# Kernel tuning notes

Measured on AMD Instinct MI355X. Metric: run time of the kernel, lower is better.

## Reference

```python
import jax, jax.numpy as jnp
import numpy as np

B, T, I, H = 128, 128, 12, 512


def setup_inputs() -> dict:
    key = jax.random.key(0)
    k1, k2, k3, k4 = jax.random.split(key, 4)
    s_ih = 1.0 / np.sqrt(H)
    return {
        "history": jax.random.normal(k1, (B, T, I), dtype=jnp.float32),
        "W_ih": jax.random.uniform(k2, (3 * H, I), dtype=jnp.float32, minval=-s_ih, maxval=s_ih),
        "W_hh": jax.random.uniform(k3, (3 * H, H), dtype=jnp.float32, minval=-s_ih, maxval=s_ih),
        "W_pred": jax.random.uniform(k4, (2, H), dtype=jnp.float32, minval=-s_ih, maxval=s_ih),
    }


def reference(history, W_ih, W_hh, W_pred):
    # GRUCell (bias=False), PyTorch gate order: r, z, n
    def step(h, x_t):
        gi = x_t @ W_ih.T            # [B, 3H]
        gh = h @ W_hh.T              # [B, 3H]
        i_r, i_z, i_n = jnp.split(gi, 3, axis=-1)
        h_r, h_z, h_n = jnp.split(gh, 3, axis=-1)
        r = jax.nn.sigmoid(i_r + h_r)
        z = jax.nn.sigmoid(i_z + h_z)
        n = jnp.tanh(i_n + r * h_n)
        h_new = (1.0 - z) * n + z * h
        logit = h_new @ W_pred.T     # per-step bubble_prediction head
        return h_new, logit

    h0 = jnp.zeros((history.shape[0], W_hh.shape[1]), dtype=history.dtype)
    xs = jnp.swapaxes(history, 0, 1)          # [T, B, I]
    h_last, logits_tbf = jax.lax.scan(step, h0, xs)
    logits = jnp.swapaxes(logits_tbf, 0, 1)   # [B, T, 2]
    return logits, h_last
```

## Files before the change

kernel.cpp:

```cpp
#include <hip/hip_runtime.h>
#include <cstdint>


typedef __attribute__((ext_vector_type(4))) float f32x4;
typedef __attribute__((ext_vector_type(8))) __bf16 bf16x8;

#define NTHREADS 256
#define CG_N 32
#define BB 16
#define HC 16
#define T_STEPS 128
#define I_DIM 12
#define H_DIM 512

#define WS_HX0   0
#define WS_HX1   262144
#define WS_FLAGS 524288

__device__ __forceinline__ float bf16f(unsigned short u){
  return __uint_as_float(((unsigned int)u) << 16);
}
__device__ __forceinline__ void split_bf16(float x, unsigned short &hi, unsigned short &lo){
  unsigned int u = __float_as_uint(x);
  hi = (unsigned short)(u >> 16);
  float r = x - __uint_as_float((u >> 16) << 16);
  unsigned int ru = __float_as_uint(r);
  ru += 0x7fffu + ((ru >> 16) & 1u);
  lo = (unsigned short)(ru >> 16);
}
__device__ __forceinline__ float fsigmoid(float x){ return 1.0f / (1.0f + __expf(-x)); }
__device__ __forceinline__ float ftanh(float x){ return 2.0f / (1.0f + __expf(-2.0f * x)) - 1.0f; }
__device__ __forceinline__ f32x4 MFMA(bf16x8 a, bf16x8 b, f32x4 c){
  return __builtin_amdgcn_mfma_f32_16x16x32_bf16(a, b, c, 0, 0, 0);
}
__device__ __forceinline__ void wait_vm0(){
  asm volatile("s_waitcnt vmcnt(0)" ::: "memory");
}
__device__ __forceinline__ unsigned int hiP(unsigned int x, unsigned int y){
  return (x >> 16) | (y & 0xFFFF0000u);
}
__device__ __forceinline__ unsigned int loP(unsigned int x, unsigned int y){
  return (x & 0xFFFFu) | (y << 16);
}

__device__ __forceinline__ void bar_lgkm(){
  asm volatile("s_waitcnt lgkmcnt(0)" ::: "memory");
  __builtin_amdgcn_sched_barrier(0);
  __builtin_amdgcn_s_barrier();
  __builtin_amdgcn_sched_barrier(0);
}
__device__ __forceinline__ void bar_raw(){
  __builtin_amdgcn_sched_barrier(0);
  __builtin_amdgcn_s_barrier();
  __builtin_amdgcn_sched_barrier(0);
}

__device__ __forceinline__ void dev_store_u32(unsigned int* p, unsigned int v){
  asm volatile("global_store_dword %0, %1, off sc1" :: "v"(p), "v"(v) : "memory");
}
__device__ __forceinline__ unsigned int dev_load_u32(const unsigned int* p){
  unsigned int v;
  asm volatile("global_load_dword %0, %1, off sc1\n\ts_waitcnt vmcnt(0)"
               : "=v"(v) : "v"(p) : "memory");
  return v;
}
__device__ __forceinline__ uint4 load4_sc1(const unsigned int* p){
  uint4 v;
  asm volatile("global_load_dwordx4 %0, %1, off sc1" : "=v"(v) : "v"(p) : "memory");
  return v;
}
__device__ __forceinline__ void load_h_row(const unsigned int* p, uint4* pr){
  uint4 v0, v1, v2, v3, v4, v5, v6, v7;
  asm volatile(
    "global_load_dwordx4 %0, %8, off sc1\n\t"
    "global_load_dwordx4 %1, %8, off offset:16 sc1\n\t"
    "global_load_dwordx4 %2, %8, off offset:32 sc1\n\t"
    "global_load_dwordx4 %3, %8, off offset:48 sc1\n\t"
    "global_load_dwordx4 %4, %8, off offset:64 sc1\n\t"
    "global_load_dwordx4 %5, %8, off offset:80 sc1\n\t"
    "global_load_dwordx4 %6, %8, off offset:96 sc1\n\t"
    "global_load_dwordx4 %7, %8, off offset:112 sc1\n\t"
    "s_waitcnt vmcnt(0)"
    : "=&v"(v0), "=&v"(v1), "=&v"(v2), "=&v"(v3),
      "=&v"(v4), "=&v"(v5), "=&v"(v6), "=&v"(v7)
    : "v"(p) : "memory");
  pr[0]=v0; pr[1]=v1; pr[2]=v2; pr[3]=v3; pr[4]=v4; pr[5]=v5; pr[6]=v6; pr[7]=v7;
}

__device__ __forceinline__ void poll_h_row(const unsigned int* p, uint4* pr,
                                           unsigned int want){
  for (;;){
    load_h_row(p, pr);
    unsigned int diff = 0u;
    #pragma unroll
    for (int b = 0; b < 8; ++b)
      diff |= (pr[b].x ^ want) | (pr[b].y ^ want) | (pr[b].z ^ want) | (pr[b].w ^ want);
    if ((diff & 3u) == 0u) break;
  }
  #pragma unroll
  for (int b = 0; b < 8; ++b){
    pr[b].x &= 0xFFFFFFFCu; pr[b].y &= 0xFFFFFFFCu;
    pr[b].z &= 0xFFFFFFFCu; pr[b].w &= 0xFFFFFFFCu;
  }
}

extern "C" __global__ void __launch_bounds__(NTHREADS, 1)
gru_persistent(const float* __restrict__ hist, const float* __restrict__ wih,
               const float* __restrict__ whh, const float* __restrict__ wpred,
               float* __restrict__ out, unsigned char* __restrict__ ws)
{
  __shared__ __align__(16) unsigned short whi_l[3*16*64*8];
  __shared__ __align__(16) unsigned short wlo_l[3*16*64*8];
  __shared__ __align__(16) unsigned short hhi_l[BB*H_DIM];
  __shared__ __align__(16) unsigned short hlo_l[BB*H_DIM];
  __shared__ __align__(16) float part_l[4*3*64*4];
  __shared__ __align__(16) float x_l[BB*I_DIM];
  __shared__ __align__(16) float wih_l[48*I_DIM];
  __shared__ __align__(16) float wpred_l[2*H_DIM];

  const int tid  = threadIdx.x;
  const int bg   = blockIdx.x & 7;
  const int cg   = blockIdx.x >> 3;
  const int wave = tid >> 6;
  const int lane = tid & 63;
  const int b_log = cg & 15;
  const int o_log = cg >> 4;

  unsigned int* hx[2] = {(unsigned int*)(ws + WS_HX0), (unsigned int*)(ws + WS_HX1)};
  unsigned int* flagsP = (unsigned int*)(ws + WS_FLAGS);

  for (int i = tid; i < 48*I_DIM; i += NTHREADS){
    int j = i / I_DIM, ii = i % I_DIM;
    int R = (j >> 4)*H_DIM + cg*HC + (j & 15);
    wih_l[i] = wih[R*I_DIM + ii];
  }
  for (int i = tid; i < 2*H_DIM; i += NTHREADS) wpred_l[i] = wpred[i];
  #pragma unroll
  for (int it = 0; it < 24; ++it){
    int f0 = (it*NTHREADS + tid) * 4;
    int j = f0 >> 9, k = f0 & 511;
    int R = (j >> 4)*H_DIM + cg*HC + (j & 15);
    float4 v = *(const float4*)(whh + R*H_DIM + k);
    int nt = j >> 4;
    int ln = (j & 15) | (((k >> 3) & 3) << 4);
    int kt = k >> 5, e = k & 7;
    int base = (((nt*16 + kt)*64) + ln)*8 + e;
    float vv[4] = {v.x, v.y, v.z, v.w};
    unsigned short h4[4], l4[4];
    #pragma unroll
    for (int q = 0; q < 4; ++q) split_bf16(vv[q], h4[q], l4[q]);
    uint2 uh, ul;
    uh.x = (unsigned int)h4[0] | ((unsigned int)h4[1] << 16);
    uh.y = (unsigned int)h4[2] | ((unsigned int)h4[3] << 16);
    ul.x = (unsigned int)l4[0] | ((unsigned int)l4[1] << 16);
    ul.y = (unsigned int)l4[2] | ((unsigned int)l4[3] << 16);
    *(uint2*)((char*)whi_l + base*2) = uh;
    *(uint2*)((char*)wlo_l + base*2) = ul;
  }

  {
    int b = tid >> 4, hc = tid & 15;
    int gidx = (bg*BB + b)*H_DIM + cg*HC + hc;
    dev_store_u32(hx[0] + gidx, 0u);
    dev_store_u32(hx[1] + gidx, 2u);
  }
  wait_vm0();
  __syncthreads();
  if (wave == 0 && lane < CG_N)
    dev_store_u32(flagsP + (bg*CG_N + lane)*CG_N + cg, 1u);
  if (wave == 0){
    const unsigned int* fp = flagsP + (bg*CG_N + cg)*CG_N + (lane & 31);
    for (;;){
      unsigned int f = dev_load_u32(fp);
      if (__ballot(f >= 1u) == ~0ull) break;
      __builtin_amdgcn_s_sleep(1);
    }
  }
  __syncthreads();

  for (int t = 0; t < T_STEPS; ++t){
    const int cur = t & 1, nxt = cur ^ 1;

    if (tid < BB*I_DIM){
      int b = tid / I_DIM, ii = tid % I_DIM;
      x_l[tid] = hist[((bg*BB + b)*T_STEPS + t)*I_DIM + ii];
    }

    {
      int row = tid & 15, col0 = (tid >> 4) * 32;
      const unsigned int* p = hx[cur] + (bg*BB + row)*H_DIM + col0;
      uint4 pr[8];
      poll_h_row(p, pr, (unsigned int)(t & 3));
      #pragma unroll
      for (int k = 0; k < 4; ++k){
        uint4 a = pr[2*k], b = pr[2*k+1];
        uint4 hi4 = { hiP(a.x,a.y), hiP(a.z,a.w), hiP(b.x,b.y), hiP(b.z,b.w) };
        uint4 lo4 = { loP(a.x,a.y), loP(a.z,a.w), loP(b.x,b.y), loP(b.z,b.w) };
        int boff = row*1024 + (((col0 + 8*k)*2) ^ ((row & 7) << 4));
        *(uint4*)((char*)hhi_l + boff) = hi4;
        *(uint4*)((char*)hlo_l + boff) = lo4;
      }
    }
    bar_lgkm();

    f32x4 acc[3];
    #pragma unroll
    for (int nt = 0; nt < 3; ++nt) acc[nt] = {0.f, 0.f, 0.f, 0.f};
    #pragma unroll
    for (int kk = 0; kk < 4; ++kk){
      int kt = wave*4 + kk;
      int arow = lane & 15;
      int aboff = arow*1024 + ((kt*64 + (lane >> 4)*16) ^ ((arow & 7) << 4));
      bf16x8 ahi = *(const bf16x8*)((const char*)hhi_l + aboff);
      bf16x8 alo = *(const bf16x8*)((const char*)hlo_l + aboff);
      #pragma unroll
      for (int nt = 0; nt < 3; ++nt){
        int bboff = (((nt*16 + kt)*64) + lane)*16;
        bf16x8 bhi = *(const bf16x8*)((const char*)whi_l + bboff);
        bf16x8 blo = *(const bf16x8*)((const char*)wlo_l + bboff);
        acc[nt] = MFMA(ahi, bhi, acc[nt]);
        acc[nt] = MFMA(ahi, blo, acc[nt]);
        acc[nt] = MFMA(alo, bhi, acc[nt]);
      }
    }
    #pragma unroll
    for (int nt = 0; nt < 3; ++nt)
      *(f32x4*)(part_l + ((wave*3 + nt)*64 + lane)*4) = acc[nt];
    bar_lgkm();

    {
      int b = tid >> 4, hc = tid & 15;
      int lc = ((b >> 2) << 4) | hc;
      int rc = b & 3;
      float gh[3];
      #pragma unroll
      for (int g = 0; g < 3; ++g){
        float s = 0.f;
        #pragma unroll
        for (int w = 0; w < 4; ++w) s += part_l[((w*3 + g)*64 + lc)*4 + rc];
        gh[g] = s;
      }
      float gi[3];
      #pragma unroll
      for (int g = 0; g < 3; ++g){
        float s = 0.f;
        #pragma unroll
        for (int ii = 0; ii < I_DIM; ++ii)
          s += x_l[b*I_DIM + ii] * wih_l[(g*16 + hc)*I_DIM + ii];
        gi[g] = s;
      }
      float r = fsigmoid(gi[0] + gh[0]);
      float z = fsigmoid(gi[1] + gh[1]);
      float n = ftanh(gi[2] + r*gh[2]);
      int colg = cg*HC + hc;
      int hoff = b*1024 + ((colg*2) ^ ((b & 7) << 4));
      float hp = bf16f(*(unsigned short*)((char*)hhi_l + hoff))
               + bf16f(*(unsigned short*)((char*)hlo_l + hoff));
      float hn = (1.0f - z)*n + z*hp;

      unsigned short shi, slo; split_bf16(hn, shi, slo);
      unsigned int pk = ((unsigned int)shi << 16) | ((unsigned int)slo & 0xFFFCu)
                      | (unsigned int)((t + 1) & 3);
      int gidx = (bg*BB + b)*H_DIM + colg;
      dev_store_u32(hx[nxt] + gidx, pk);
      if (t == T_STEPS - 1) out[32768 + gidx] = hn;
    }

    if (wave == 0 && t > 0){
      int c = lane * 8;
      int boff = b_log*1024 + ((c*2) ^ ((b_log & 7) << 4));
      uint4 vh = *(const uint4*)((const char*)hhi_l + boff);
      uint4 vl = *(const uint4*)((const char*)hlo_l + boff);
      const unsigned short* ph = (const unsigned short*)&vh;
      const unsigned short* pl = (const unsigned short*)&vl;
      float p = 0.f;
      #pragma unroll
      for (int e = 0; e < 8; ++e)
        p += (bf16f(ph[e]) + bf16f(pl[e])) * wpred_l[o_log*H_DIM + c + e];
      #pragma unroll
      for (int m = 1; m < 64; m <<= 1) p += __shfl_xor(p, m);
      if (lane == 0) out[((bg*BB + b_log)*T_STEPS + (t-1))*2 + o_log] = p;
    }

    bar_raw();
  }

  if (wave == 0){
    const unsigned int* p = hx[0] + (bg*BB + b_log)*H_DIM + lane*8;
    uint4 a0, a1;
    for (;;){
      a0 = load4_sc1(p); a1 = load4_sc1(p + 4);
      wait_vm0();
      unsigned int diff = (a0.x | a0.y | a0.z | a0.w | a1.x | a1.y | a1.z | a1.w);
      if ((((a0.x ^ 0u) | (a0.y) | (a0.z) | (a0.w) | a1.x | a1.y | a1.z | a1.w) & 3u) == 0u) break;
      (void)diff;
      __builtin_amdgcn_s_sleep(1);
    }
    const unsigned int pk8[8] = {a0.x & 0xFFFFFFFCu, a0.y & 0xFFFFFFFCu,
                                 a0.z & 0xFFFFFFFCu, a0.w & 0xFFFFFFFCu,
                                 a1.x & 0xFFFFFFFCu, a1.y & 0xFFFFFFFCu,
                                 a1.z & 0xFFFFFFFCu, a1.w & 0xFFFFFFFCu};
    float pacc = 0.f;
    #pragma unroll
    for (int e = 0; e < 8; ++e){
      unsigned int v = pk8[e];
      float hv = bf16f((unsigned short)(v >> 16)) + bf16f((unsigned short)(v & 0xFFFFu));
      pacc += hv * wpred_l[o_log*H_DIM + lane*8 + e];
    }
    #pragma unroll
    for (int m = 1; m < 64; m <<= 1) pacc += __shfl_xor(pacc, m);
    if (lane == 0) out[((bg*BB + b_log)*T_STEPS + 127)*2 + o_log] = pacc;
  }
}

extern "C" void kernel_launch(void* const* d_in, const int* in_sizes, int n_in,
                              void* d_out, int out_size, void* d_ws, size_t ws_size,
                              hipStream_t stream) {
  const float* hist  = (const float*)d_in[0];
  const float* wih   = (const float*)d_in[1];
  const float* whh   = (const float*)d_in[2];
  const float* wpred = (const float*)d_in[3];
  float* out = (float*)d_out;
  unsigned char* ws = (unsigned char*)d_ws;

  hipMemsetAsync(ws + WS_FLAGS, 0, 8*CG_N*CG_N*4, stream);

  gru_persistent<<<dim3(256), dim3(NTHREADS), 0, stream>>>(hist, wih, whh, wpred, out, ws);
}
```

Baseline: 524.5 us.

## Split each GRU timestep into two half-batch phases to overlap cross-block waits

Each timestep now polls, computes and publishes the hidden state in two halves of 8 batch rows instead of one 16-row pass. Work on the first half can start as soon as those rows arrive from other blocks, so the inter-block wait overlaps with the other half's computation. The input tile is double-buffered and the trailing per-step barrier is removed. In exchange, the full 16-row MFMA tile is computed twice per step, half of it on stale rows, and each step now has more barriers.

After: 529.9 us. About the same (+1.0%).

```diff
diff --git a/kernel.cpp b/kernel.cpp
--- a/kernel.cpp
+++ b/kernel.cpp
@@ -8,6 +8,7 @@
 #define NTHREADS 256
 #define CG_N 32
 #define BB 16
+#define BBH 8
 #define HC 16
 #define T_STEPS 128
 #define I_DIM 12
@@ -49,11 +50,6 @@
   __builtin_amdgcn_s_barrier();
   __builtin_amdgcn_sched_barrier(0);
 }
-__device__ __forceinline__ void bar_raw(){
-  __builtin_amdgcn_sched_barrier(0);
-  __builtin_amdgcn_s_barrier();
-  __builtin_amdgcn_sched_barrier(0);
-}
 
 __device__ __forceinline__ void dev_store_u32(unsigned int* p, unsigned int v){
   asm volatile("global_store_dword %0, %1, off sc1" :: "v"(p), "v"(v) : "memory");
@@ -69,36 +65,30 @@
   asm volatile("global_load_dwordx4 %0, %1, off sc1" : "=v"(v) : "v"(p) : "memory");
   return v;
 }
-__device__ __forceinline__ void load_h_row(const unsigned int* p, uint4* pr){
-  uint4 v0, v1, v2, v3, v4, v5, v6, v7;
+__device__ __forceinline__ void load_h4(const unsigned int* p, uint4* pr){
+  uint4 v0, v1, v2, v3;
   asm volatile(
-    "global_load_dwordx4 %0, %8, off sc1\n\t"
-    "global_load_dwordx4 %1, %8, off offset:16 sc1\n\t"
-    "global_load_dwordx4 %2, %8, off offset:32 sc1\n\t"
-    "global_load_dwordx4 %3, %8, off offset:48 sc1\n\t"
-    "global_load_dwordx4 %4, %8, off offset:64 sc1\n\t"
-    "global_load_dwordx4 %5, %8, off offset:80 sc1\n\t"
-    "global_load_dwordx4 %6, %8, off offset:96 sc1\n\t"
-    "global_load_dwordx4 %7, %8, off offset:112 sc1\n\t"
+    "global_load_dwordx4 %0, %4, off sc1\n\t"
+    "global_load_dwordx4 %1, %4, off offset:16 sc1\n\t"
+    "global_load_dwordx4 %2, %4, off offset:32 sc1\n\t"
+    "global_load_dwordx4 %3, %4, off offset:48 sc1\n\t"
     "s_waitcnt vmcnt(0)"
-    : "=&v"(v0), "=&v"(v1), "=&v"(v2), "=&v"(v3),
-      "=&v"(v4), "=&v"(v5), "=&v"(v6), "=&v"(v7)
+    : "=&v"(v0), "=&v"(v1), "=&v"(v2), "=&v"(v3)
     : "v"(p) : "memory");
-  pr[0]=v0; pr[1]=v1; pr[2]=v2; pr[3]=v3; pr[4]=v4; pr[5]=v5; pr[6]=v6; pr[7]=v7;
-}
-
-__device__ __forceinline__ void poll_h_row(const unsigned int* p, uint4* pr,
-                                           unsigned int want){
+  pr[0]=v0; pr[1]=v1; pr[2]=v2; pr[3]=v3;
+}
+__device__ __forceinline__ void poll_h4(const unsigned int* p, uint4* pr,
+                                        unsigned int want){
   for (;;){
-    load_h_row(p, pr);
+    load_h4(p, pr);
     unsigned int diff = 0u;
     #pragma unroll
-    for (int b = 0; b < 8; ++b)
+    for (int b = 0; b < 4; ++b)
       diff |= (pr[b].x ^ want) | (pr[b].y ^ want) | (pr[b].z ^ want) | (pr[b].w ^ want);
     if ((diff & 3u) == 0u) break;
   }
   #pragma unroll
-  for (int b = 0; b < 8; ++b){
+  for (int b = 0; b < 4; ++b){
     pr[b].x &= 0xFFFFFFFCu; pr[b].y &= 0xFFFFFFFCu;
     pr[b].z &= 0xFFFFFFFCu; pr[b].w &= 0xFFFFFFFCu;
   }
@@ -114,7 +104,7 @@
   __shared__ __align__(16) unsigned short hhi_l[BB*H_DIM];
   __shared__ __align__(16) unsigned short hlo_l[BB*H_DIM];
   __shared__ __align__(16) float part_l[4*3*64*4];
-  __shared__ __align__(16) float x_l[BB*I_DIM];
+  __shared__ __align__(16) float x_l[2][BB*I_DIM];
   __shared__ __align__(16) float wih_l[48*I_DIM];
   __shared__ __align__(16) float wpred_l[2*H_DIM];
 
@@ -178,111 +168,117 @@
   }
   __syncthreads();
 
+  const int prow = tid & 7;
+  const int pc0  = (tid >> 3) * 16;
+
   for (int t = 0; t < T_STEPS; ++t){
     const int cur = t & 1, nxt = cur ^ 1;
+    const unsigned int wantT = (unsigned int)(t & 3);
 
     if (tid < BB*I_DIM){
       int b = tid / I_DIM, ii = tid % I_DIM;
-      x_l[tid] = hist[((bg*BB + b)*T_STEPS + t)*I_DIM + ii];
-    }
-
-    {
-      int row = tid & 15, col0 = (tid >> 4) * 32;
-      const unsigned int* p = hx[cur] + (bg*BB + row)*H_DIM + col0;
-      uint4 pr[8];
-      poll_h_row(p, pr, (unsigned int)(t & 3));
+      x_l[cur][tid] = hist[((bg*BB + b)*T_STEPS + t)*I_DIM + ii];
+    }
+
+    #pragma unroll
+    for (int half = 0; half < 2; ++half){
+      const int ro = half * BBH;
+      {
+        int lrow = ro + prow;
+        const unsigned int* p = hx[cur] + (bg*BB + lrow)*H_DIM + pc0;
+        uint4 pr[4];
+        poll_h4(p, pr, wantT);
+        #pragma unroll
+        for (int k = 0; k < 2; ++k){
+          uint4 a = pr[2*k], b = pr[2*k+1];
+          uint4 hi4 = { hiP(a.x,a.y), hiP(a.z,a.w), hiP(b.x,b.y), hiP(b.z,b.w) };
+          uint4 lo4 = { loP(a.x,a.y), loP(a.z,a.w), loP(b.x,b.y), loP(b.z,b.w) };
+          int boff = lrow*1024 + (((pc0 + 8*k)*2) ^ ((lrow & 7) << 4));
+          *(uint4*)((char*)hhi_l + boff) = hi4;
+          *(uint4*)((char*)hlo_l + boff) = lo4;
+        }
+      }
+      bar_lgkm();
+
+      f32x4 acc[3];
       #pragma unroll
-      for (int k = 0; k < 4; ++k){
-        uint4 a = pr[2*k], b = pr[2*k+1];
-        uint4 hi4 = { hiP(a.x,a.y), hiP(a.z,a.w), hiP(b.x,b.y), hiP(b.z,b.w) };
-        uint4 lo4 = { loP(a.x,a.y), loP(a.z,a.w), loP(b.x,b.y), loP(b.z,b.w) };
-        int boff = row*1024 + (((col0 + 8*k)*2) ^ ((row & 7) << 4));
-        *(uint4*)((char*)hhi_l + boff) = hi4;
-        *(uint4*)((char*)hlo_l + boff) = lo4;
+      for (int nt = 0; nt < 3; ++nt) acc[nt] = {0.f, 0.f, 0.f, 0.f};
+      #pragma unroll
+      for (int kk = 0; kk < 4; ++kk){
+        int kt = wave*4 + kk;
+        int arow = lane & 15;
+        int aboff = arow*1024 + ((kt*64 + (lane >> 4)*16) ^ ((arow & 7) << 4));
+        bf16x8 ahi = *(const bf16x8*)((const char*)hhi_l + aboff);
+        bf16x8 alo = *(const bf16x8*)((const char*)hlo_l + aboff);
+        #pragma unroll
+        for (int nt = 0; nt < 3; ++nt){
+          int bboff = (((nt*16 + kt)*64) + lane)*16;
+          bf16x8 bhi = *(const bf16x8*)((const char*)whi_l + bboff);
+          bf16x8 blo = *(const bf16x8*)((const char*)wlo_l + bboff);
+          acc[nt] = MFMA(ahi, bhi, acc[nt]);
+          acc[nt] = MFMA(ahi, blo, acc[nt]);
+          acc[nt] = MFMA(alo, bhi, acc[nt]);
+        }
       }
-    }
-    bar_lgkm();
-
-    f32x4 acc[3];
-    #pragma unroll
-    for (int nt = 0; nt < 3; ++nt) acc[nt] = {0.f, 0.f, 0.f, 0.f};
-    #pragma unroll
-    for (int kk = 0; kk < 4; ++kk){
-      int kt = wave*4 + kk;
-      int arow = lane & 15;
-      int aboff = arow*1024 + ((kt*64 + (lane >> 4)*16) ^ ((arow & 7) << 4));
-      bf16x8 ahi = *(const bf16x8*)((const char*)hhi_l + aboff);
-      bf16x8 alo = *(const bf16x8*)((const char*)hlo_l + aboff);
       #pragma unroll
-      for (int nt = 0; nt < 3; ++nt){
-        int bboff = (((nt*16 + kt)*64) + lane)*16;
-        bf16x8 bhi = *(const bf16x8*)((const char*)whi_l + bboff);
-        bf16x8 blo = *(const bf16x8*)((const char*)wlo_l + bboff);
-        acc[nt] = MFMA(ahi, bhi, acc[nt]);
-        acc[nt] = MFMA(ahi, blo, acc[nt]);
-        acc[nt] = MFMA(alo, bhi, acc[nt]);
+      for (int nt = 0; nt < 3; ++nt)
+        *(f32x4*)(part_l + ((wave*3 + nt)*64 + lane)*4) = acc[nt];
+      bar_lgkm();
+
+      if (tid < BBH*HC){
+        int b = ro + (tid >> 4), hc = tid & 15;
+        int lc = ((b >> 2) << 4) | hc;
+        int rc = b & 3;
+        float gh[3];
+        #pragma unroll
+        for (int g = 0; g < 3; ++g){
+          float s = 0.f;
+          #pragma unroll
+          for (int w = 0; w < 4; ++w) s += part_l[((w*3 + g)*64 + lc)*4 + rc];
+          gh[g] = s;
+        }
+        float gi[3];
+        #pragma unroll
+        for (int g = 0; g < 3; ++g){
+          float s = 0.f;
+          #pragma unroll
+          for (int ii = 0; ii < I_DIM; ++ii)
+            s += x_l[cur][b*I_DIM + ii] * wih_l[(g*16 + hc)*I_DIM + ii];
+          gi[g] = s;
+        }
+        float r = fsigmoid(gi[0] + gh[0]);
+        float z = fsigmoid(gi[1] + gh[1]);
+        float n = ftanh(gi[2] + r*gh[2]);
+        int colg = cg*HC + hc;
+        int hoff = b*1024 + ((colg*2) ^ ((b & 7) << 4));
+        float hp = bf16f(*(unsigned short*)((char*)hhi_l + hoff))
+                 + bf16f(*(unsigned short*)((char*)hlo_l + hoff));
+        float hn = (1.0f - z)*n + z*hp;
+
+        unsigned short shi, slo; split_bf16(hn, shi, slo);
+        unsigned int pk = ((unsigned int)shi << 16) | ((unsigned int)slo & 0xFFFCu)
+                        | (unsigned int)((t + 1) & 3);
+        int gidx = (bg*BB + b)*H_DIM + colg;
+        dev_store_u32(hx[nxt] + gidx, pk);
+        if (t == T_STEPS - 1) out[32768 + gidx] = hn;
       }
-    }
-    #pragma unroll
-    for (int nt = 0; nt < 3; ++nt)
-      *(f32x4*)(part_l + ((wave*3 + nt)*64 + lane)*4) = acc[nt];
-    bar_lgkm();
-
-    {
-      int b = tid >> 4, hc = tid & 15;
-      int lc = ((b >> 2) << 4) | hc;
-      int rc = b & 3;
-      float gh[3];
-      #pragma unroll
-      for (int g = 0; g < 3; ++g){
-        float s = 0.f;
-        #pragma unroll
-        for (int w = 0; w < 4; ++w) s += part_l[((w*3 + g)*64 + lc)*4 + rc];
-        gh[g] = s;
+
+      if (wave == 0 && t > 0 && (b_log >> 3) == half){
+        int c = lane * 8;
+        int boff = b_log*1024 + ((c*2) ^ ((b_log & 7) << 4));
+        uint4 vh = *(const uint4*)((const char*)hhi_l + boff);
+        uint4 vl = *(const uint4*)((const char*)hlo_l + boff);
+        const unsigned short* ph = (const unsigned short*)&vh;
+        const unsigned short* pl = (const unsigned short*)&vl;
+        float p = 0.f;
+        #pragma unroll
+        for (int e = 0; e < 8; ++e)
+          p += (bf16f(ph[e]) + bf16f(pl[e])) * wpred_l[o_log*H_DIM + c + e];
+        #pragma unroll
+        for (int m = 1; m < 64; m <<= 1) p += __shfl_xor(p, m);
+        if (lane == 0) out[((bg*BB + b_log)*T_STEPS + (t-1))*2 + o_log] = p;
       }
-      float gi[3];
-      #pragma unroll
-      for (int g = 0; g < 3; ++g){
-        float s = 0.f;
-        #pragma unroll
-        for (int ii = 0; ii < I_DIM; ++ii)
-          s += x_l[b*I_DIM + ii] * wih_l[(g*16 + hc)*I_DIM + ii];
-        gi[g] = s;
-      }
-      float r = fsigmoid(gi[0] + gh[0]);
-      float z = fsigmoid(gi[1] + gh[1]);
-      float n = ftanh(gi[2] + r*gh[2]);
-      int colg = cg*HC + hc;
-      int hoff = b*1024 + ((colg*2) ^ ((b & 7) << 4));
-      float hp = bf16f(*(unsigned short*)((char*)hhi_l + hoff))
-               + bf16f(*(unsigned short*)((char*)hlo_l + hoff));
-      float hn = (1.0f - z)*n + z*hp;
-
-      unsigned short shi, slo; split_bf16(hn, shi, slo);
-      unsigned int pk = ((unsigned int)shi << 16) | ((unsigned int)slo & 0xFFFCu)
-                      | (unsigned int)((t + 1) & 3);
-      int gidx = (bg*BB + b)*H_DIM + colg;
-      dev_store_u32(hx[nxt] + gidx, pk);
-      if (t == T_STEPS - 1) out[32768 + gidx] = hn;
-    }
-
-    if (wave == 0 && t > 0){
-      int c = lane * 8;
-      int boff = b_log*1024 + ((c*2) ^ ((b_log & 7) << 4));
-      uint4 vh = *(const uint4*)((const char*)hhi_l + boff);
-      uint4 vl = *(const uint4*)((const char*)hlo_l + boff);
-      const unsigned short* ph = (const unsigned short*)&vh;
-      const unsigned short* pl = (const unsigned short*)&vl;
-      float p = 0.f;
-      #pragma unroll
-      for (int e = 0; e < 8; ++e)
-        p += (bf16f(ph[e]) + bf16f(pl[e])) * wpred_l[o_log*H_DIM + c + e];
-      #pragma unroll
-      for (int m = 1; m < 64; m <<= 1) p += __shfl_xor(p, m);
-      if (lane == 0) out[((bg*BB + b_log)*T_STEPS + (t-1))*2 + o_log] = p;
-    }
-
-    bar_raw();
+    }
   }
 
   if (wave == 0){
@@ -291,9 +287,7 @@
     for (;;){
       a0 = load4_sc1(p); a1 = load4_sc1(p + 4);
       wait_vm0();
-      unsigned int diff = (a0.x | a0.y | a0.z | a0.w | a1.x | a1.y | a1.z | a1.w);
-      if ((((a0.x ^ 0u) | (a0.y) | (a0.z) | (a0.w) | a1.x | a1.y | a1.z | a1.w) & 3u) == 0u) break;
-      (void)diff;
+      if (((a0.x | a0.y | a0.z | a0.w | a1.x | a1.y | a1.z | a1.w) & 3u) == 0u) break;
       __builtin_amdgcn_s_sleep(1);
     }
     const unsigned int pk8[8] = {a0.x & 0xFFFFFFFCu, a0.y & 0xFFFFFFFCu,
```

## Split workgroup into two independent wave pairs with LDS flag synchronization

Applied to the files above, without the earlier changes.

The block's four waves are split into two pairs. Each pair polls and updates its own 8 of the 16 batch rows, and the two waves in a pair meet through workgroup-scope atomic flags in LDS instead of full-block s_barriers. The goal is to let each half of the batch advance as soon as its own hidden-state rows arrive, rather than waiting on the slowest row in the whole block. The cost is that each wave now runs twice as many MFMA K-tiles, because every pair computes all 16 rows. The pairs also spin on LDS flags and read the other half's possibly stale rows, which they never use. The prediction weights are additionally trimmed to the single output row this block needs.

Measured after the change: 904.6 us. +72.5%, slower.

```diff
diff --git a/kernel.cpp b/kernel.cpp
--- a/kernel.cpp
+++ b/kernel.cpp
@@ -8,6 +8,7 @@
 #define NTHREADS 256
 #define CG_N 32
 #define BB 16
+#define BBH 8
 #define HC 16
 #define T_STEPS 128
 #define I_DIM 12
@@ -41,18 +42,6 @@
 }
 __device__ __forceinline__ unsigned int loP(unsigned int x, unsigned int y){
   return (x & 0xFFFFu) | (y << 16);
-}
-
-__device__ __forceinline__ void bar_lgkm(){
-  asm volatile("s_waitcnt lgkmcnt(0)" ::: "memory");
-  __builtin_amdgcn_sched_barrier(0);
-  __builtin_amdgcn_s_barrier();
-  __builtin_amdgcn_sched_barrier(0);
-}
-__device__ __forceinline__ void bar_raw(){
-  __builtin_amdgcn_sched_barrier(0);
-  __builtin_amdgcn_s_barrier();
-  __builtin_amdgcn_sched_barrier(0);
 }
 
 __device__ __forceinline__ void dev_store_u32(unsigned int* p, unsigned int v){
@@ -86,7 +75,6 @@
     : "v"(p) : "memory");
   pr[0]=v0; pr[1]=v1; pr[2]=v2; pr[3]=v3; pr[4]=v4; pr[5]=v5; pr[6]=v6; pr[7]=v7;
 }
-
 __device__ __forceinline__ void poll_h_row(const unsigned int* p, uint4* pr,
                                            unsigned int want){
   for (;;){
@@ -116,25 +104,31 @@
   __shared__ __align__(16) float part_l[4*3*64*4];
   __shared__ __align__(16) float x_l[BB*I_DIM];
   __shared__ __align__(16) float wih_l[48*I_DIM];
-  __shared__ __align__(16) float wpred_l[2*H_DIM];
+  __shared__ __align__(16) float wpred_l[H_DIM];
+  __shared__ int sync_l[2][2];
 
   const int tid  = threadIdx.x;
   const int bg   = blockIdx.x & 7;
   const int cg   = blockIdx.x >> 3;
   const int wave = tid >> 6;
   const int lane = tid & 63;
+  const int c    = wave >> 1;
+  const int cw   = wave & 1;
+  const int ctid = cw*64 + lane;
+  const int ro   = c * BBH;
   const int b_log = cg & 15;
   const int o_log = cg >> 4;
 
   unsigned int* hx[2] = {(unsigned int*)(ws + WS_HX0), (unsigned int*)(ws + WS_HX1)};
   unsigned int* flagsP = (unsigned int*)(ws + WS_FLAGS);
 
+  if (tid < 4) sync_l[tid >> 1][tid & 1] = 0;
   for (int i = tid; i < 48*I_DIM; i += NTHREADS){
     int j = i / I_DIM, ii = i % I_DIM;
     int R = (j >> 4)*H_DIM + cg*HC + (j & 15);
     wih_l[i] = wih[R*I_DIM + ii];
   }
-  for (int i = tid; i < 2*H_DIM; i += NTHREADS) wpred_l[i] = wpred[i];
+  for (int i = tid; i < H_DIM; i += NTHREADS) wpred_l[i] = wpred[o_log*H_DIM + i];
   #pragma unroll
   for (int it = 0; it < 24; ++it){
     int f0 = (it*NTHREADS + tid) * 4;
@@ -178,37 +172,49 @@
   }
   __syncthreads();
 
+  int* fl = &sync_l[c][0];
+  auto pair_sync = [&](int gen){
+    asm volatile("s_waitcnt lgkmcnt(0)" ::: "memory");
+    if (lane == 0)
+      __hip_atomic_store(&fl[cw], gen, __ATOMIC_RELEASE, __HIP_MEMORY_SCOPE_WORKGROUP);
+    while (__hip_atomic_load(&fl[cw^1], __ATOMIC_ACQUIRE, __HIP_MEMORY_SCOPE_WORKGROUP) < gen)
+      ;
+  };
+
+  const int prow = ctid & 7;
+  const int pc0  = (ctid >> 3) * 32;
+
   for (int t = 0; t < T_STEPS; ++t){
     const int cur = t & 1, nxt = cur ^ 1;
-
-    if (tid < BB*I_DIM){
-      int b = tid / I_DIM, ii = tid % I_DIM;
-      x_l[tid] = hist[((bg*BB + b)*T_STEPS + t)*I_DIM + ii];
-    }
+    const unsigned int wantT = (unsigned int)(t & 3);
 
     {
-      int row = tid & 15, col0 = (tid >> 4) * 32;
-      const unsigned int* p = hx[cur] + (bg*BB + row)*H_DIM + col0;
+      int lrow = ro + prow;
+      const unsigned int* p = hx[cur] + (bg*BB + lrow)*H_DIM + pc0;
       uint4 pr[8];
-      poll_h_row(p, pr, (unsigned int)(t & 3));
+      poll_h_row(p, pr, wantT);
       #pragma unroll
       for (int k = 0; k < 4; ++k){
         uint4 a = pr[2*k], b = pr[2*k+1];
         uint4 hi4 = { hiP(a.x,a.y), hiP(a.z,a.w), hiP(b.x,b.y), hiP(b.z,b.w) };
         uint4 lo4 = { loP(a.x,a.y), loP(a.z,a.w), loP(b.x,b.y), loP(b.z,b.w) };
-        int boff = row*1024 + (((col0 + 8*k)*2) ^ ((row & 7) << 4));
+        int boff = lrow*1024 + (((pc0 + 8*k)*2) ^ ((lrow & 7) << 4));
         *(uint4*)((char*)hhi_l + boff) = hi4;
         *(uint4*)((char*)hlo_l + boff) = lo4;
       }
-    }
-    bar_lgkm();
+      if (ctid < BBH*I_DIM){
+        int b = ro + ctid/I_DIM, ii = ctid % I_DIM;
+        x_l[b*I_DIM + ii] = hist[((bg*BB + b)*T_STEPS + t)*I_DIM + ii];
+      }
+    }
+    pair_sync(3*t + 1);
 
     f32x4 acc[3];
     #pragma unroll
     for (int nt = 0; nt < 3; ++nt) acc[nt] = {0.f, 0.f, 0.f, 0.f};
     #pragma unroll
-    for (int kk = 0; kk < 4; ++kk){
-      int kt = wave*4 + kk;
+    for (int kk = 0; kk < 8; ++kk){
+      int kt = cw*8 + kk;
       int arow = lane & 15;
       int aboff = arow*1024 + ((kt*64 + (lane >> 4)*16) ^ ((arow & 7) << 4));
       bf16x8 ahi = *(const bf16x8*)((const char*)hhi_l + aboff);
@@ -226,18 +232,19 @@
     #pragma unroll
     for (int nt = 0; nt < 3; ++nt)
       *(f32x4*)(part_l + ((wave*3 + nt)*64 + lane)*4) = acc[nt];
-    bar_lgkm();
+    pair_sync(3*t + 2);
 
     {
-      int b = tid >> 4, hc = tid & 15;
-      int lc = ((b >> 2) << 4) | hc;
+      int b = ro + (ctid >> 4), hc = ctid & 15;
+      int lc = hc + 16*(b >> 2);
       int rc = b & 3;
       float gh[3];
       #pragma unroll
       for (int g = 0; g < 3; ++g){
         float s = 0.f;
         #pragma unroll
-        for (int w = 0; w < 4; ++w) s += part_l[((w*3 + g)*64 + lc)*4 + rc];
+        for (int w = 0; w < 2; ++w)
+          s += part_l[(((c*2 + w)*3 + g)*64 + lc)*4 + rc];
         gh[g] = s;
       }
       float gi[3];
@@ -266,9 +273,9 @@
       if (t == T_STEPS - 1) out[32768 + gidx] = hn;
     }
 
-    if (wave == 0 && t > 0){
-      int c = lane * 8;
-      int boff = b_log*1024 + ((c*2) ^ ((b_log & 7) << 4));
+    if (cw == 0 && t > 0 && (b_log >> 3) == c){
+      int col = lane * 8;
+      int boff = b_log*1024 + ((col*2) ^ ((b_log & 7) << 4));
       uint4 vh = *(const uint4*)((const char*)hhi_l + boff);
       uint4 vl = *(const uint4*)((const char*)hlo_l + boff);
       const unsigned short* ph = (const unsigned short*)&vh;
@@ -276,13 +283,13 @@
       float p = 0.f;
       #pragma unroll
       for (int e = 0; e < 8; ++e)
-        p += (bf16f(ph[e]) + bf16f(pl[e])) * wpred_l[o_log*H_DIM + c + e];
+        p += (bf16f(ph[e]) + bf16f(pl[e])) * wpred_l[col + e];
       #pragma unroll
       for (int m = 1; m < 64; m <<= 1) p += __shfl_xor(p, m);
       if (lane == 0) out[((bg*BB + b_log)*T_STEPS + (t-1))*2 + o_log] = p;
     }
 
-    bar_raw();
+    pair_sync(3*t + 3);
   }
 
   if (wave == 0){
@@ -291,9 +298,7 @@
     for (;;){
       a0 = load4_sc1(p); a1 = load4_sc1(p + 4);
       wait_vm0();
-      unsigned int diff = (a0.x | a0.y | a0.z | a0.w | a1.x | a1.y | a1.z | a1.w);
-      if ((((a0.x ^ 0u) | (a0.y) | (a0.z) | (a0.w) | a1.x | a1.y | a1.z | a1.w) & 3u) == 0u) break;
-      (void)diff;
+      if (((a0.x | a0.y | a0.z | a0.w | a1.x | a1.y | a1.z | a1.w) & 3u) == 0u) break;
       __builtin_amdgcn_s_sleep(1);
     }
     const unsigned int pk8[8] = {a0.x & 0xFFFFFFFCu, a0.y & 0xFFFFFFFCu,
@@ -305,7 +310,7 @@
     for (int e = 0; e < 8; ++e){
       unsigned int v = pk8[e];
       float hv = bf16f((unsigned short)(v >> 16)) + bf16f((unsigned short)(v & 0xFFFFu));
-      pacc += hv * wpred_l[o_log*H_DIM + lane*8 + e];
+      pacc += hv * wpred_l[lane*8 + e];
     }
     #pragma unroll
     for (int m = 1; m < 64; m <<= 1) pacc += __shfl_xor(pacc, m);
```
